# Optimization experiments

Hardware: AMD Instinct MI355X
Metric: run time of the kernel (lower is better)

The kernel has to match this reference:

```python
import jax, jax.numpy as jnp
import numpy as np

BLOCK_M = 64
BLOCK_K = 64
THRES = 0.8


def setup_inputs() -> dict:
    key = jax.random.key(0)
    k1, k2 = jax.random.split(key)
    bsz, d_in, d_out = 8192, 4096, 4096
    x = jax.random.normal(k1, (bsz, d_in), dtype=jnp.float32)
    # kaiming_uniform_(a=sqrt(5)) on a (d_in, d_out) tensor -> bound = 1/sqrt(d_out)
    bound = 1.0 / np.sqrt(d_out)
    weight = jax.random.uniform(k2, (d_in, d_out), dtype=jnp.float32,
                                minval=-bound, maxval=bound)
    return {"x": x, "weight": weight}


def reference(x, weight):
    bsz, hidden = x.shape
    nm, nk = bsz // BLOCK_M, hidden // BLOCK_K
    # per-block average magnitude of activations: [nm, nk]
    blocks = jnp.abs(x).reshape(nm, BLOCK_M, nk, BLOCK_K)
    avg_mag = blocks.mean(axis=(1, 3))
    block_mask = avg_mag > THRES  # [nm, nk] bool
    # expand mask to element level and zero inactive activation blocks
    mask_elem = jnp.repeat(jnp.repeat(block_mask, BLOCK_M, axis=0), BLOCK_K, axis=1)
    x_masked = jnp.where(mask_elem, x, 0.0)
    # block-sparse masked GEMM (dense reference of the same math)
    return x_masked @ weight
```

## Files before the change

kernel.cpp:

```cpp
#include <hip/hip_runtime.h>
#include <hip/hip_bf16.h>
#include <stdint.h>

#define BSZ   8192
#define D_IN  4096
#define D_OUT 4096
#define NM    128
#define NK    64

typedef __bf16 bf16x8 __attribute__((ext_vector_type(8)));
typedef float  f32x4  __attribute__((ext_vector_type(4)));
typedef unsigned short ushort_t;

__device__ __forceinline__ ushort_t f2bf(float f) {
  union { __hip_bfloat16 h; ushort_t u; } c;
  c.h = __float2bfloat16(f);
  return c.u;
}

__device__ __forceinline__ bf16x8 ld_frag(const ushort_t* p) {
  union { uint4 u; bf16x8 b; } cv;
  cv.u = *(const uint4*)p;
  return cv.b;
}

__device__ __forceinline__ void glds16(const ushort_t* g, ushort_t* l) {
  __builtin_amdgcn_global_load_lds(
      (const __attribute__((address_space(1))) unsigned int*)g,
      (__attribute__((address_space(3))) unsigned int*)l,
      16, 0, 0);
}

__global__ __launch_bounds__(256) void mask_cast_kernel(
    const float* __restrict__ x, ushort_t* __restrict__ xb,
    int* __restrict__ mask) {
  const int kblk = blockIdx.x;
  const int mblk = blockIdx.y;
  const int tid  = threadIdx.x;
  const size_t row0 = (size_t)mblk * 64;
  const int    col0 = kblk * 64;

  float4 v[4];
  double s = 0.0;
#pragma unroll
  for (int i = 0; i < 4; ++i) {
    int j = i * 256 + tid;
    int r = j >> 4;
    int c = (j & 15) * 4;
    v[i] = *(const float4*)(x + (row0 + r) * D_IN + col0 + c);
    s += (double)fabsf(v[i].x) + (double)fabsf(v[i].y) +
         (double)fabsf(v[i].z) + (double)fabsf(v[i].w);
  }

  __shared__ double red[256];
  __shared__ int mflag;
  red[tid] = s;
  __syncthreads();
  for (int off = 128; off > 0; off >>= 1) {
    if (tid < off) red[tid] += red[tid + off];
    __syncthreads();
  }
  if (tid == 0) {
    float avg = (float)(red[0] * (1.0 / 4096.0));
    int m = (avg > 0.8f) ? 1 : 0;
    mflag = m;
    mask[mblk * NK + kblk] = m;
  }
  __syncthreads();
  const int act = mflag;

#pragma unroll
  for (int i = 0; i < 4; ++i) {
    int j = i * 256 + tid;
    int r = j >> 4;
    int c = (j & 15) * 4;
    ushort_t o0 = 0, o1 = 0, o2 = 0, o3 = 0;
    if (act) {
      o0 = f2bf(v[i].x); o1 = f2bf(v[i].y);
      o2 = f2bf(v[i].z); o3 = f2bf(v[i].w);
    }
    ushort4 o = make_ushort4(o0, o1, o2, o3);
    *(ushort4*)(xb + (row0 + r) * D_IN + col0 + c) = o;
  }
}

__global__ __launch_bounds__(256) void wcast_transpose_kernel(
    const float* __restrict__ w, ushort_t* __restrict__ wT) {
  const int ntile = blockIdx.x;
  const int ktile = blockIdx.y;
  const int tid   = threadIdx.x;
  const int k0 = ktile * 64, n0 = ntile * 64;

  __shared__ ushort_t t[64][65];

#pragma unroll
  for (int i = 0; i < 4; ++i) {
    int j = i * 256 + tid;
    int r = j >> 4;
    int c = (j & 15) * 4;
    float4 v = *(const float4*)(w + (size_t)(k0 + r) * D_OUT + n0 + c);
    t[r][c + 0] = f2bf(v.x);
    t[r][c + 1] = f2bf(v.y);
    t[r][c + 2] = f2bf(v.z);
    t[r][c + 3] = f2bf(v.w);
  }
  __syncthreads();
#pragma unroll
  for (int i = 0; i < 4; ++i) {
    int j = i * 256 + tid;
    int r = j >> 4;
    int c = (j & 15) * 4;
    ushort4 o = make_ushort4(t[c + 0][r], t[c + 1][r], t[c + 2][r], t[c + 3][r]);
    *(ushort4*)(wT + (size_t)(n0 + r) * D_IN + k0 + c) = o;
  }
}

__global__ __launch_bounds__(256) void bsp_gemm_kernel(
    const ushort_t* __restrict__ xb, const ushort_t* __restrict__ wT,
    const int* __restrict__ mask, float* __restrict__ out) {
  const int ntile = blockIdx.x;
  const int mblk  = blockIdx.y;
  const int tid   = threadIdx.x;
  const int lane  = tid & 63;
  const int wv    = tid >> 6;
  const int m0 = mblk * 64;
  const int n0 = ntile * 256;

  __shared__ ushort_t As[64 * 64];
  __shared__ ushort_t Bs[256 * 64];
  __shared__ int nact;
  __shared__ unsigned char klist[64];

  const int* mrow = mask + mblk * NK;
  if (tid == 0) {
    int n = 0;
#pragma unroll
    for (int kb = 0; kb < NK; ++kb) {
      if (mrow[kb] != 0) klist[n++] = (unsigned char)kb;
    }
    nact = n;
  }
  __syncthreads();
  const int na = nact;

  f32x4 acc[4][4] = {};

  const int lr  = lane >> 3;
  const int lc  = (lane & 7) * 8;
  const int q   = lane >> 4;
  const int l15 = lane & 15;

  for (int ki = 0; ki < na; ++ki) {
    const int kb = klist[ki];
    const int k0 = kb * 64;

#pragma unroll
    for (int t = 0; t < 2; ++t) {
      int rb = wv * 16 + t * 8;
      glds16(xb + (size_t)(m0 + rb + lr) * D_IN + k0 + lc, &As[rb * 64]);
    }
#pragma unroll
    for (int t = 0; t < 8; ++t) {
      int rb = wv * 64 + t * 8;
      glds16(wT + (size_t)(n0 + rb + lr) * D_IN + k0 + lc, &Bs[rb * 64]);
    }
    __syncthreads();

#pragma unroll
    for (int c = 0; c < 2; ++c) {
      bf16x8 a[4], b[4];
#pragma unroll
      for (int i = 0; i < 4; ++i)
        a[i] = ld_frag(&As[(i * 16 + l15) * 64 + c * 32 + q * 8]);
#pragma unroll
      for (int j = 0; j < 4; ++j)
        b[j] = ld_frag(&Bs[(wv * 64 + j * 16 + l15) * 64 + c * 32 + q * 8]);
#pragma unroll
      for (int i = 0; i < 4; ++i)
#pragma unroll
        for (int j = 0; j < 4; ++j)
          acc[i][j] = __builtin_amdgcn_mfma_f32_16x16x32_bf16(
              a[i], b[j], acc[i][j], 0, 0, 0);
    }
    __syncthreads();
  }

#pragma unroll
  for (int i = 0; i < 4; ++i) {
#pragma unroll
    for (int j = 0; j < 4; ++j) {
#pragma unroll
      for (int r = 0; r < 4; ++r) {
        int row = m0 + i * 16 + q * 4 + r;
        int col = n0 + wv * 64 + j * 16 + l15;
        out[(size_t)row * D_OUT + col] = acc[i][j][r];
      }
    }
  }
}

extern "C" void kernel_launch(void* const* d_in, const int* in_sizes, int n_in,
                              void* d_out, int out_size, void* d_ws, size_t ws_size,
                              hipStream_t stream) {
  const float* x = (const float*)d_in[0];
  const float* w = (const float*)d_in[1];

  ushort_t* xb  = (ushort_t*)d_ws;
  ushort_t* wT  = (ushort_t*)((char*)d_ws + (size_t)BSZ * D_IN * 2);
  int*      msk = (int*)((char*)d_ws + (size_t)BSZ * D_IN * 2 + (size_t)D_IN * D_OUT * 2);
  float*    out = (float*)d_out;

  hipLaunchKernelGGL(mask_cast_kernel, dim3(NK, NM), dim3(256), 0, stream,
                     x, xb, msk);
  hipLaunchKernelGGL(wcast_transpose_kernel, dim3(64, 64), dim3(256), 0, stream,
                     w, wT);
  hipLaunchKernelGGL(bsp_gemm_kernel, dim3(D_OUT / 256, NM), dim3(256), 0, stream,
                     xb, wT, msk, out);
}
```

Measured before the change: 471.0 us.

## Swizzle GEMM LDS tiles, use shuffle reduction, skip stores for inactive blocks

The GEMM now loads A and B tiles into LDS with an XOR swizzle on 16-byte chunks (chunk index XOR row mod 8). It reads MFMA fragments with the matching swizzle, which is meant to remove the LDS bank conflicts caused by the 128-byte row stride. The mask/cast kernel replaces its shared-memory tree reduction with wavefront shuffles plus a 4-entry cross-wave sum. It also stops writing zero bf16 values for inactive blocks, which relies on the GEMM never reading those workspace regions. That leaves those regions of the workspace uninitialized.

```diff
diff --git a/kernel.cpp b/kernel.cpp
--- a/kernel.cpp
+++ b/kernel.cpp
@@ -37,6 +37,8 @@
   const int kblk = blockIdx.x;
   const int mblk = blockIdx.y;
   const int tid  = threadIdx.x;
+  const int lane = tid & 63;
+  const int wv   = tid >> 6;
   const size_t row0 = (size_t)mblk * 64;
   const int    col0 = kblk * 64;
 
@@ -52,35 +54,38 @@
          (double)fabsf(v[i].z) + (double)fabsf(v[i].w);
   }
 
-  __shared__ double red[256];
+#pragma unroll
+  for (int off = 32; off > 0; off >>= 1) {
+    union { double d; int i2[2]; } u;
+    u.d = s;
+    u.i2[0] = __shfl_xor(u.i2[0], off, 64);
+    u.i2[1] = __shfl_xor(u.i2[1], off, 64);
+    s += u.d;
+  }
+
+  __shared__ double wsum[4];
   __shared__ int mflag;
-  red[tid] = s;
-  __syncthreads();
-  for (int off = 128; off > 0; off >>= 1) {
-    if (tid < off) red[tid] += red[tid + off];
-    __syncthreads();
-  }
+  if (lane == 0) wsum[wv] = s;
+  __syncthreads();
   if (tid == 0) {
-    float avg = (float)(red[0] * (1.0 / 4096.0));
+    double tot = wsum[0] + wsum[1] + wsum[2] + wsum[3];
+    float avg = (float)(tot * (1.0 / 4096.0));
     int m = (avg > 0.8f) ? 1 : 0;
     mflag = m;
     mask[mblk * NK + kblk] = m;
   }
   __syncthreads();
-  const int act = mflag;
-
-#pragma unroll
-  for (int i = 0; i < 4; ++i) {
-    int j = i * 256 + tid;
-    int r = j >> 4;
-    int c = (j & 15) * 4;
-    ushort_t o0 = 0, o1 = 0, o2 = 0, o3 = 0;
-    if (act) {
-      o0 = f2bf(v[i].x); o1 = f2bf(v[i].y);
-      o2 = f2bf(v[i].z); o3 = f2bf(v[i].w);
-    }
-    ushort4 o = make_ushort4(o0, o1, o2, o3);
-    *(ushort4*)(xb + (row0 + r) * D_IN + col0 + c) = o;
+
+  if (mflag) {
+#pragma unroll
+    for (int i = 0; i < 4; ++i) {
+      int j = i * 256 + tid;
+      int r = j >> 4;
+      int c = (j & 15) * 4;
+      ushort4 o = make_ushort4(f2bf(v[i].x), f2bf(v[i].y),
+                               f2bf(v[i].z), f2bf(v[i].w));
+      *(ushort4*)(xb + (row0 + r) * D_IN + col0 + c) = o;
+    }
   }
 }
 
@@ -146,9 +151,10 @@
   f32x4 acc[4][4] = {};
 
   const int lr  = lane >> 3;
-  const int lc  = (lane & 7) * 8;
+  const int lcs = ((lane & 7) ^ (lane >> 3)) * 8;
   const int q   = lane >> 4;
   const int l15 = lane & 15;
+  const int sx  = l15 & 7;
 
   for (int ki = 0; ki < na; ++ki) {
     const int kb = klist[ki];
@@ -157,24 +163,25 @@
 #pragma unroll
     for (int t = 0; t < 2; ++t) {
       int rb = wv * 16 + t * 8;
-      glds16(xb + (size_t)(m0 + rb + lr) * D_IN + k0 + lc, &As[rb * 64]);
+      glds16(xb + (size_t)(m0 + rb + lr) * D_IN + k0 + lcs, &As[rb * 64]);
     }
 #pragma unroll
     for (int t = 0; t < 8; ++t) {
       int rb = wv * 64 + t * 8;
-      glds16(wT + (size_t)(n0 + rb + lr) * D_IN + k0 + lc, &Bs[rb * 64]);
+      glds16(wT + (size_t)(n0 + rb + lr) * D_IN + k0 + lcs, &Bs[rb * 64]);
     }
     __syncthreads();
 
 #pragma unroll
     for (int c = 0; c < 2; ++c) {
+      const int sw = ((c * 4 + q) ^ sx) * 8;
       bf16x8 a[4], b[4];
 #pragma unroll
       for (int i = 0; i < 4; ++i)
-        a[i] = ld_frag(&As[(i * 16 + l15) * 64 + c * 32 + q * 8]);
+        a[i] = ld_frag(&As[(i * 16 + l15) * 64 + sw]);
 #pragma unroll
       for (int j = 0; j < 4; ++j)
-        b[j] = ld_frag(&Bs[(wv * 64 + j * 16 + l15) * 64 + c * 32 + q * 8]);
+        b[j] = ld_frag(&Bs[(wv * 64 + j * 16 + l15) * 64 + sw]);
 #pragma unroll
       for (int i = 0; i < 4; ++i)
 #pragma unroll
```

New measurement: 440.3 us. 1.07x faster.
